# Performance work log

Hardware: AMD Instinct MI355X
Metric: run time of the kernel (lower is better)

## Reference

```python
import jax, jax.numpy as jnp
import numpy as np

BATCH = 128
BUFFER_SIZE = 16
H, W, C = 128, 128, 3


def setup_inputs() -> dict:
    key = jax.random.key(0)
    k1, _ = jax.random.split(key)
    inputs = jax.random.normal(k1, (BATCH, H, W, C), dtype=jnp.float32)
    # Initial buffer state (keras.backend.zeros in build())
    buffer = jnp.zeros((BUFFER_SIZE, H, W, C), dtype=jnp.float32)
    return {"inputs": inputs, "buffer": buffer}


def reference(inputs, buffer):
    # Sequential semantics of the original loop:
    #   for i in range(batch):
    #       buffer = concat([buffer[1:], inputs[i:i+1]], axis=0)
    #       output[i] = buffer
    # Unrolled, with combined = concat([buffer0, inputs], axis=0):
    #   output[i] = combined[i+1 : i+1+buffer_size]
    # which is a vectorized sliding-window gather (no Python loop).
    K = buffer.shape[0]                      # buffer_size
    B = inputs.shape[0]                      # batch
    combined = jnp.concatenate([buffer, inputs], axis=0)   # [K+B, H, W, C]
    idx = jnp.arange(B)[:, None] + 1 + jnp.arange(K)[None, :]  # [B, K]
    out = combined[idx]                      # [B, K, H, W, C]
    return out
```

## Files before the change

### kernel.cpp

```cpp
#include <hip/hip_runtime.h>


constexpr int BATCH     = 128;
constexpr int KBUF      = 16;
constexpr int FRAME_F32 = 128 * 128 * 3;
constexpr int FRAME_F4  = FRAME_F32 / 4;
constexpr int BLOCK     = 256;
constexpr int CHUNKS    = FRAME_F4 / BLOCK;

__global__ __launch_bounds__(BLOCK)
void ImageBuffer_86784109183359_kernel(const float4* __restrict__ inputs,
                                       const float4* __restrict__ buffer,
                                       float4* __restrict__ out) {
    const int bid   = blockIdx.x;
    const int frame = bid / CHUNKS;
    const int chunk = bid % CHUNKS;
    const int off   = chunk * BLOCK + threadIdx.x;

    const int b = frame >> 4;
    const int k = frame & 15;
    const int j = b + 1 + k;

    const float4* __restrict__ src =
        (j < KBUF) ? (buffer + (size_t)j * FRAME_F4)
                   : (inputs + (size_t)(j - KBUF) * FRAME_F4);

    out[(size_t)frame * FRAME_F4 + off] = src[off];
}

extern "C" void kernel_launch(void* const* d_in, const int* in_sizes, int n_in,
                              void* d_out, int out_size, void* d_ws, size_t ws_size,
                              hipStream_t stream) {
    const float4* inputs = (const float4*)d_in[0];
    const float4* buffer = (const float4*)d_in[1];
    float4* out = (float4*)d_out;

    const int n_frames = BATCH * KBUF;
    const int grid = n_frames * CHUNKS;

    ImageBuffer_86784109183359_kernel<<<grid, BLOCK, 0, stream>>>(inputs, buffer, out);
}
```

Before: 412.4 us.

## Read each source frame once and scatter it to all output slots

```diff
diff --git a/kernel.cpp b/kernel.cpp
--- a/kernel.cpp
+++ b/kernel.cpp
@@ -1,42 +1,54 @@
 #include <hip/hip_runtime.h>
 
+
+typedef float f32x4 __attribute__((ext_vector_type(4)));
 
 constexpr int BATCH     = 128;
 constexpr int KBUF      = 16;
 constexpr int FRAME_F32 = 128 * 128 * 3;
 constexpr int FRAME_F4  = FRAME_F32 / 4;
 constexpr int BLOCK     = 256;
-constexpr int CHUNKS    = FRAME_F4 / BLOCK;
+constexpr int VEC       = 2;
+constexpr int CHUNK_F4  = BLOCK * VEC;
+constexpr int CHUNKS    = FRAME_F4 / CHUNK_F4;
+constexpr int NSRC      = BATCH + KBUF - 1;
 
 __global__ __launch_bounds__(BLOCK)
-void ImageBuffer_86784109183359_kernel(const float4* __restrict__ inputs,
-                                       const float4* __restrict__ buffer,
-                                       float4* __restrict__ out) {
-    const int bid   = blockIdx.x;
-    const int frame = bid / CHUNKS;
-    const int chunk = bid % CHUNKS;
-    const int off   = chunk * BLOCK + threadIdx.x;
+void ImageBuffer_86784109183359_kernel(const f32x4* __restrict__ inputs,
+                                       const f32x4* __restrict__ buffer,
+                                       f32x4* __restrict__ out) {
+    const int j     = blockIdx.x / CHUNKS + 1;
+    const int chunk = blockIdx.x % CHUNKS;
+    const int off   = chunk * CHUNK_F4 + threadIdx.x;
 
-    const int b = frame >> 4;
-    const int k = frame & 15;
-    const int j = b + 1 + k;
-
-    const float4* __restrict__ src =
+    const f32x4* __restrict__ src =
         (j < KBUF) ? (buffer + (size_t)j * FRAME_F4)
                    : (inputs + (size_t)(j - KBUF) * FRAME_F4);
 
-    out[(size_t)frame * FRAME_F4 + off] = src[off];
+    const f32x4 v0 = __builtin_nontemporal_load(&src[off]);
+    const f32x4 v1 = __builtin_nontemporal_load(&src[off + BLOCK]);
+
+    const int b_lo = (j > KBUF) ? (j - KBUF) : 0;
+    const int b_hi = (j - 1 < BATCH - 1) ? (j - 1) : (BATCH - 1);
+
+    size_t base = (size_t)(15 * b_lo + j - 1) * FRAME_F4 + off;
+    const size_t stride = (size_t)15 * FRAME_F4;
+
+    for (int b = b_lo; b <= b_hi; ++b) {
+        __builtin_nontemporal_store(v0, &out[base]);
+        __builtin_nontemporal_store(v1, &out[base + BLOCK]);
+        base += stride;
+    }
 }
 
 extern "C" void kernel_launch(void* const* d_in, const int* in_sizes, int n_in,
                               void* d_out, int out_size, void* d_ws, size_t ws_size,
                               hipStream_t stream) {
-    const float4* inputs = (const float4*)d_in[0];
-    const float4* buffer = (const float4*)d_in[1];
-    float4* out = (float4*)d_out;
+    const f32x4* inputs = (const f32x4*)d_in[0];
+    const f32x4* buffer = (const f32x4*)d_in[1];
+    f32x4* out = (f32x4*)d_out;
 
-    const int n_frames = BATCH * KBUF;
-    const int grid = n_frames * CHUNKS;
+    const int grid = NSRC * CHUNKS;
 
     ImageBuffer_86784109183359_kernel<<<grid, BLOCK, 0, stream>>>(inputs, buffer, out);
 }
```

After: 409.8 us. About the same (-0.6%).
